# Performance work log

Measured on AMD Instinct MI355X. Metric: run time of the kernel, lower is better.

The kernel has to match this reference:

```python
import jax, jax.numpy as jnp
import numpy as np
import math

BASE_RES = 16
MAX_RES = 2048
LEVELS = 16
FEAT_DIM = 2
LOG_B = math.log(MAX_RES / BASE_RES) / (LEVELS - 1)  # per-level log scale


def setup_inputs() -> dict:
    key = jax.random.key(0)
    k1, k2 = jax.random.split(key)
    B = 1048576
    positions = jax.random.uniform(k1, (B, 3), dtype=jnp.float32)
    total = MAX_RES * MAX_RES * 3 * FEAT_DIM
    # torch.nn.init.uniform_ -> U[0,1)
    plane_table = jax.random.uniform(k2, (total,), dtype=jnp.float32)
    return {"positions": positions, "plane_table": plane_table}


def _encode(positions, plane_table):
    B = positions.shape[0]
    dtype = positions.dtype
    # planes: (xy, yz, zx) -> [B, 3 planes, 2 coords]
    x, y, z = positions[:, 0], positions[:, 1], positions[:, 2]
    xyz6 = jnp.stack([x, y, y, z, z, x], axis=1).reshape(B, 3, 2)
    planes = plane_table.reshape(3, MAX_RES * MAX_RES, FEAT_DIM)
    plane_ids = jnp.arange(3)  # [3]
    outs = []
    for level in range(LEVELS):
        scale = BASE_RES * math.exp(level * LOG_B) - 1.0
        res = int(math.ceil(scale)) + 1  # grid_resolution
        pos = xyz6 * (res - 1) + 0.5            # [B,3,2]
        pg = jnp.floor(pos)
        frac = pos - pg                          # fractional part
        pg = pg.astype(jnp.int32)
        local = jnp.zeros((B, 3, FEAT_DIM), dtype)
        for idx in range(4):  # 4 bilinear corners
            w = jnp.ones((B, 3), dtype)
            coords = []
            for d in range(2):
                if idx & (1 << d):
                    coords.append(pg[..., d] + 1)
                    w = w * frac[..., d]
                else:
                    coords.append(pg[..., d])
                    w = w * (1.0 - frac[..., d])
            c = jnp.stack(coords, axis=-1).astype(dtype)  # [B,3,2]
            # remap corner from level grid to the max_res storage grid (truncating cast)
            c_ori = (c / res * (MAX_RES - 1)).astype(jnp.int32)
            index = c_ori[..., 0] + c_ori[..., 1] * MAX_RES  # [B,3] flat plane index
            feats = planes[plane_ids[None, :], index]        # [B,3,FEAT_DIM] gather
            local = local + w[..., None] * feats
        # cross-plane product
        outs.append(local[:, 0] * local[:, 1] * local[:, 2])  # [B,FEAT_DIM]
    out = jnp.stack(outs, axis=2)  # [B, FEAT_DIM, LEVELS]; sn = j*LEVELS + level
    return out.reshape(B, FEAT_DIM * LEVELS)


def reference(positions, plane_table):
    return _encode(positions, plane_table)
```

## Files before the change

### kernel.cpp

```cpp
#include <hip/hip_runtime.h>
#include <math.h>

#define LEVELS 16
#define MAX_RES 2048
#define NCELL_BITS 5
#define NCELLS (1 << (3 * NCELL_BITS))
#define LC_LO 9
#define LC_HI 12

typedef float nfloat4 __attribute__((ext_vector_type(4)));

struct ResParams {
  int res[LEVELS];
  int coff[LEVELS];
  int S[LEVELS];
};


__device__ __forceinline__ unsigned int morton5(int cx, int cy, int cz) {
  unsigned int k = 0;
  #pragma unroll
  for (int b = 0; b < NCELL_BITS; ++b)
    k |= (((cx >> b) & 1) << (3 * b)) | (((cy >> b) & 1) << (3 * b + 1)) |
         (((cz >> b) & 1) << (3 * b + 2));
  return k;
}

__device__ __forceinline__ unsigned int cell_of(float x, float y, float z) {
  int cx = min(31, max(0, (int)(x * 32.0f)));
  int cy = min(31, max(0, (int)(y * 32.0f)));
  int cz = min(31, max(0, (int)(z * 32.0f)));
  return morton5(cx, cy, cz);
}

__global__ __launch_bounds__(256) void keys_hist(const float* __restrict__ pos,
                                                 unsigned int* __restrict__ hist, int B) {
  int i = blockIdx.x * 256 + threadIdx.x;
  if (i >= B) return;
  atomicAdd(&hist[cell_of(pos[i*3], pos[i*3+1], pos[i*3+2])], 1u);
}

__global__ __launch_bounds__(1024) void scan_kernel(const unsigned int* __restrict__ hist,
                                                    unsigned int* __restrict__ offs) {
  __shared__ unsigned int part[1024];
  const int SEG = NCELLS / 1024;
  int t = threadIdx.x;
  int base = t * SEG;
  unsigned int s = 0;
  #pragma unroll
  for (int j = 0; j < SEG; ++j) s += hist[base + j];
  part[t] = s;
  __syncthreads();
  for (int off = 1; off < 1024; off <<= 1) {
    unsigned int v = (t >= off) ? part[t - off] : 0u;
    __syncthreads();
    part[t] += v;
    __syncthreads();
  }
  unsigned int run = part[t] - s;
  #pragma unroll
  for (int j = 0; j < SEG; ++j) {
    unsigned int c = hist[base + j];
    offs[base + j] = run;
    run += c;
  }
}

__global__ __launch_bounds__(256) void scatter_kernel(const float* __restrict__ pos,
                                                      unsigned int* __restrict__ offs,
                                                      nfloat4* __restrict__ sorted, int B) {
  int i = blockIdx.x * 256 + threadIdx.x;
  if (i >= B) return;
  float x = pos[i*3], y = pos[i*3+1], z = pos[i*3+2];
  unsigned int slot = atomicAdd(&offs[cell_of(x, y, z)], 1u);
  nfloat4 v = {x, y, z, __int_as_float(i)};
  sorted[slot] = v;
}

__global__ __launch_bounds__(256) void build_compact(const float* __restrict__ table,
                                                     float2* __restrict__ compact,
                                                     ResParams P) {
  int l = LC_LO + blockIdx.y;
  int S = P.S[l];
  int e = blockIdx.x * 256 + threadIdx.x;
  if (e >= 3 * S) return;
  int res = P.res[l];
  int W = res + 1;
  int p = e / S;
  int rem = e - p * S;
  int v = rem / W;
  int u = rem - v * W;
  const float fres = (float)res;
  int cu = (int)(__fmul_rn(__fdiv_rn((float)u, fres), 2047.0f));
  int cv = (int)(__fmul_rn(__fdiv_rn((float)v, fres), 2047.0f));
  const float* plane = table + (size_t)p * (MAX_RES * MAX_RES * 2);
  compact[P.coff[l] + e] = *reinterpret_cast<const float2*>(plane + (size_t)(cu + (cv << 11)) * 2);
}


template <bool USE_COMPACT>
__global__ __launch_bounds__(256) void triplane_main(
    const nfloat4* __restrict__ sorted,
    const float* __restrict__ table,
    const float2* __restrict__ compact,
    float* __restrict__ out,
    ResParams P, int B, int nwg)
{
  int wg = blockIdx.x;
  int q = nwg >> 3, r = nwg & 7;
  int xcd = wg & 7, idx = wg >> 3;
  int swz = (xcd < r) ? xcd * (q + 1) + idx : r * (q + 1) + (xcd - r) * q + idx;
  int t = swz * 256 + (int)threadIdx.x;
  if (t >= B) return;

  nfloat4 s = sorted[t];
  float x = s.x, y = s.y, z = s.z;
  int orig = __float_as_int(s.w);

  float uarr[3] = {x, y, z};
  float varr[3] = {y, z, x};

  float o0[LEVELS], o1[LEVELS];

  #pragma unroll
  for (int l = 0; l < LEVELS; ++l) {
    const int   res   = P.res[l];
    const float resm1 = (float)(res - 1);
    const float fres  = (float)res;
    const bool  cpath = USE_COMPACT && (l >= LC_LO && l <= LC_HI);

    float prod0 = 1.0f, prod1 = 1.0f;

    #pragma unroll
    for (int p = 0; p < 3; ++p) {
      float pu = __fadd_rn(__fmul_rn(uarr[p], resm1), 0.5f);
      float pv = __fadd_rn(__fmul_rn(varr[p], resm1), 0.5f);
      float gu = floorf(pu), gv = floorf(pv);
      float fu = __fsub_rn(pu, gu);
      float fv = __fsub_rn(pv, gv);

      float f00x, f00y, f10x, f10y, f01x, f01y, f11x, f11y;

      if (cpath) {
        int iu = (int)gu, iv = (int)gv;
        int W = res + 1;
        const float2* lv = compact + (P.coff[l] + p * P.S[l]);
        int i0 = iv * W + iu;
        const nfloat4 r0 = *reinterpret_cast<const nfloat4*>(lv + i0);
        const nfloat4 r1 = *reinterpret_cast<const nfloat4*>(lv + i0 + W);
        f00x = r0.x; f00y = r0.y; f10x = r0.z; f10y = r0.w;
        f01x = r1.x; f01y = r1.y; f11x = r1.z; f11y = r1.w;
      } else {
        float gu1 = __fadd_rn(gu, 1.0f);
        float gv1 = __fadd_rn(gv, 1.0f);
        int cou0 = (int)(__fmul_rn(__fdiv_rn(gu,  fres), 2047.0f));
        int cou1 = (int)(__fmul_rn(__fdiv_rn(gu1, fres), 2047.0f));
        int cov0 = (int)(__fmul_rn(__fdiv_rn(gv,  fres), 2047.0f));
        int cov1 = (int)(__fmul_rn(__fdiv_rn(gv1, fres), 2047.0f));

        const float* plane = table + (size_t)p * (MAX_RES * MAX_RES * 2);

        if (l == 15) {
          const nfloat4 r0 = *reinterpret_cast<const nfloat4*>(plane + (size_t)(cou0 + (cov0 << 11)) * 2);
          const nfloat4 r1 = *reinterpret_cast<const nfloat4*>(plane + (size_t)(cou0 + (cov1 << 11)) * 2);
          const bool adj = (cou1 != cou0);
          f00x = r0.x; f00y = r0.y;
          f10x = adj ? r0.z : r0.x;  f10y = adj ? r0.w : r0.y;
          f01x = r1.x; f01y = r1.y;
          f11x = adj ? r1.z : r1.x;  f11y = adj ? r1.w : r1.y;
        } else {
          const float2 f00 = *reinterpret_cast<const float2*>(plane + (size_t)(cou0 + (cov0 << 11)) * 2);
          const float2 f10 = *reinterpret_cast<const float2*>(plane + (size_t)(cou1 + (cov0 << 11)) * 2);
          const float2 f01 = *reinterpret_cast<const float2*>(plane + (size_t)(cou0 + (cov1 << 11)) * 2);
          const float2 f11 = *reinterpret_cast<const float2*>(plane + (size_t)(cou1 + (cov1 << 11)) * 2);
          f00x = f00.x; f00y = f00.y; f10x = f10.x; f10y = f10.y;
          f01x = f01.x; f01y = f01.y; f11x = f11.x; f11y = f11.y;
        }
      }

      float w00 = (1.0f - fu) * (1.0f - fv);
      float w10 = fu * (1.0f - fv);
      float w01 = (1.0f - fu) * fv;
      float w11 = fu * fv;

      float a0 = 0.0f, a1 = 0.0f;
      a0 += w00 * f00x;  a1 += w00 * f00y;
      a0 += w10 * f10x;  a1 += w10 * f10y;
      a0 += w01 * f01x;  a1 += w01 * f01y;
      a0 += w11 * f11x;  a1 += w11 * f11y;

      prod0 *= a0;
      prod1 *= a1;
    }

    o0[l] = prod0;
    o1[l] = prod1;
  }

  nfloat4* base = reinterpret_cast<nfloat4*>(out + (size_t)orig * 32);
  #pragma unroll
  for (int k = 0; k < 4; ++k) {
    nfloat4 v0 = {o0[k*4+0], o0[k*4+1], o0[k*4+2], o0[k*4+3]};
    nfloat4 v1 = {o1[k*4+0], o1[k*4+1], o1[k*4+2], o1[k*4+3]};
    base[k] = v0;
    base[4 + k] = v1;
  }
}

extern "C" void kernel_launch(void* const* d_in, const int* in_sizes, int n_in,
                              void* d_out, int out_size, void* d_ws, size_t ws_size,
                              hipStream_t stream) {
  const float* positions = (const float*)d_in[0];
  const float* table     = (const float*)d_in[1];
  float* out             = (float*)d_out;
  int B = in_sizes[0] / 3;

  ResParams P;
  const double LOG_B = log(2048.0 / 16.0) / (double)(LEVELS - 1);
  int runoff = 0, Smax = 0;
  for (int l = 0; l < LEVELS; ++l) {
    double scale = 16.0 * exp((double)l * LOG_B) - 1.0;
    P.res[l] = (int)ceil(scale) + 1;
    P.coff[l] = 0; P.S[l] = 0;
  }
  for (int l = LC_LO; l <= LC_HI; ++l) {
    int W = P.res[l] + 1;
    P.S[l] = W * W;
    P.coff[l] = runoff;
    runoff += 3 * P.S[l];
    if (P.S[l] > Smax) Smax = P.S[l];
  }

  int nwg = (B + 255) / 256;

  size_t off_hist    = 0;
  size_t off_offs    = off_hist + (size_t)NCELLS * 4;
  size_t off_sorted  = off_offs + (size_t)NCELLS * 4;
  size_t off_compact = off_sorted + (size_t)B * 16;
  size_t need_sort   = off_compact;
  size_t need_all    = off_compact + (size_t)runoff * 8;

  if (ws_size < need_sort) return;

  unsigned int* hist = (unsigned int*)((char*)d_ws + off_hist);
  unsigned int* offs = (unsigned int*)((char*)d_ws + off_offs);
  nfloat4*      srt  = (nfloat4*)((char*)d_ws + off_sorted);
  float2*       cmp  = (float2*)((char*)d_ws + off_compact);

  hipMemsetAsync(hist, 0, (size_t)NCELLS * 4, stream);
  hipLaunchKernelGGL(keys_hist, dim3(nwg), dim3(256), 0, stream, positions, hist, B);
  hipLaunchKernelGGL(scan_kernel, dim3(1), dim3(1024), 0, stream, hist, offs);
  hipLaunchKernelGGL(scatter_kernel, dim3(nwg), dim3(256), 0, stream, positions, offs, srt, B);

  if (ws_size >= need_all) {
    int nx = (3 * Smax + 255) / 256;
    int ny = LC_HI - LC_LO + 1;
    hipLaunchKernelGGL(build_compact, dim3(nx, ny), dim3(256), 0, stream, table, cmp, P);
    hipLaunchKernelGGL((triplane_main<true>), dim3(nwg), dim3(256), 0, stream,
                       srt, table, cmp, out, P, B, nwg);
  } else {
    hipLaunchKernelGGL((triplane_main<false>), dim3(nwg), dim3(256), 0, stream,
                       srt, table, cmp, out, P, B, nwg);
  }
}
```

Measured before the change: 465.4 us.

## Stage table rows in LDS for compact build and use nontemporal loads/stores

The compact-table build now gives each block one storage row of one plane. The block loads the full 2048-entry row coalesced into shared memory and then gathers the downsampled columns from LDS, replacing per-element scattered global reads. The main kernel reads sorted positions and writes its output with nontemporal hints to reduce cache pollution. Each block reads a whole row even though only W columns are used, so more bytes are read in exchange for coalesced access.

```diff
diff --git a/kernel.cpp b/kernel.cpp
--- a/kernel.cpp
+++ b/kernel.cpp
@@ -9,6 +9,7 @@
 #define LC_HI 12
 
 typedef float nfloat4 __attribute__((ext_vector_type(4)));
+typedef float nfloat2 __attribute__((ext_vector_type(2)));
 
 struct ResParams {
   int res[LEVELS];
@@ -80,21 +81,34 @@
 __global__ __launch_bounds__(256) void build_compact(const float* __restrict__ table,
                                                      float2* __restrict__ compact,
                                                      ResParams P) {
+  __shared__ nfloat2 rowbuf[MAX_RES];
   int l = LC_LO + blockIdx.y;
-  int S = P.S[l];
-  int e = blockIdx.x * 256 + threadIdx.x;
-  if (e >= 3 * S) return;
   int res = P.res[l];
   int W = res + 1;
-  int p = e / S;
-  int rem = e - p * S;
-  int v = rem / W;
-  int u = rem - v * W;
+  int bx = blockIdx.x;
+  if (bx >= 3 * W) return;
+  int p = bx / W;
+  int v = bx - p * W;
   const float fres = (float)res;
-  int cu = (int)(__fmul_rn(__fdiv_rn((float)u, fres), 2047.0f));
+
   int cv = (int)(__fmul_rn(__fdiv_rn((float)v, fres), 2047.0f));
-  const float* plane = table + (size_t)p * (MAX_RES * MAX_RES * 2);
-  compact[P.coff[l] + e] = *reinterpret_cast<const float2*>(plane + (size_t)(cu + (cv << 11)) * 2);
+  const float* src = table + (size_t)p * (MAX_RES * MAX_RES * 2) + (size_t)(cv << 11) * 2;
+
+  const nfloat4* src4 = reinterpret_cast<const nfloat4*>(src);
+  #pragma unroll
+  for (int j = (int)threadIdx.x; j < MAX_RES / 2; j += 256) {
+    nfloat4 r = src4[j];
+    rowbuf[j * 2]     = nfloat2{r.x, r.y};
+    rowbuf[j * 2 + 1] = nfloat2{r.z, r.w};
+  }
+  __syncthreads();
+
+  float2* dst = compact + (P.coff[l] + p * P.S[l] + v * W);
+  for (int u = (int)threadIdx.x; u < W; u += 256) {
+    int cu = (int)(__fmul_rn(__fdiv_rn((float)u, fres), 2047.0f));
+    nfloat2 e = rowbuf[cu];
+    dst[u] = make_float2(e.x, e.y);
+  }
 }
 
 
@@ -113,7 +127,7 @@
   int t = swz * 256 + (int)threadIdx.x;
   if (t >= B) return;
 
-  nfloat4 s = sorted[t];
+  nfloat4 s = __builtin_nontemporal_load(sorted + t);
   float x = s.x, y = s.y, z = s.z;
   int orig = __float_as_int(s.w);
 
@@ -202,8 +216,8 @@
   for (int k = 0; k < 4; ++k) {
     nfloat4 v0 = {o0[k*4+0], o0[k*4+1], o0[k*4+2], o0[k*4+3]};
     nfloat4 v1 = {o1[k*4+0], o1[k*4+1], o1[k*4+2], o1[k*4+3]};
-    base[k] = v0;
-    base[4 + k] = v1;
+    __builtin_nontemporal_store(v0, base + k);
+    __builtin_nontemporal_store(v1, base + 4 + k);
   }
 }
 
@@ -217,7 +231,7 @@
 
   ResParams P;
   const double LOG_B = log(2048.0 / 16.0) / (double)(LEVELS - 1);
-  int runoff = 0, Smax = 0;
+  int runoff = 0, Wmax = 0;
   for (int l = 0; l < LEVELS; ++l) {
     double scale = 16.0 * exp((double)l * LOG_B) - 1.0;
     P.res[l] = (int)ceil(scale) + 1;
@@ -228,7 +242,7 @@
     P.S[l] = W * W;
     P.coff[l] = runoff;
     runoff += 3 * P.S[l];
-    if (P.S[l] > Smax) Smax = P.S[l];
+    if (W > Wmax) Wmax = W;
   }
 
   int nwg = (B + 255) / 256;
@@ -253,9 +267,8 @@
   hipLaunchKernelGGL(scatter_kernel, dim3(nwg), dim3(256), 0, stream, positions, offs, srt, B);
 
   if (ws_size >= need_all) {
-    int nx = (3 * Smax + 255) / 256;
     int ny = LC_HI - LC_LO + 1;
-    hipLaunchKernelGGL(build_compact, dim3(nx, ny), dim3(256), 0, stream, table, cmp, P);
+    hipLaunchKernelGGL(build_compact, dim3(3 * Wmax, ny), dim3(256), 0, stream, table, cmp, P);
     hipLaunchKernelGGL((triplane_main<true>), dim3(nwg), dim3(256), 0, stream,
                        srt, table, cmp, out, P, B, nwg);
   } else {
```

Result: slower. 629.5 us (+35.3%).
